# Kernel optimization log

Measured on AMD Instinct MI355X. Metric: run time of the kernel, lower is better.

Reference implementation:

```python
import jax, jax.numpy as jnp
import numpy as np

N = 100000          # nodes
E = 800000          # directed edges (before self-loops)
IN_C = 3
HID = 48            # out_channels per head
HEADS = 4
NUM_LAYERS = 3
NEG_SLOPE = 0.2     # PyG GATv2Conv default negative_slope


def setup_inputs() -> dict:
    key = jax.random.key(0)
    ks = iter(jax.random.split(key, 64))
    inp = {}
    inp["x"] = jax.random.normal(next(ks), (N, IN_C), dtype=jnp.float32)
    inp["edge_index"] = jax.random.randint(next(ks), (2, E), 0, N, dtype=jnp.int32)
    dins = [IN_C] + [HID] * (NUM_LAYERS - 1)
    for l, din in enumerate(dins):
        s = 1.0 / np.sqrt(din)
        inp[f"Wl{l}"] = (jax.random.normal(next(ks), (din, HEADS * HID)) * s).astype(jnp.float32)
        inp[f"bl{l}"] = jnp.zeros((HEADS * HID,), jnp.float32)
        inp[f"Wr{l}"] = (jax.random.normal(next(ks), (din, HEADS * HID)) * s).astype(jnp.float32)
        inp[f"br{l}"] = jnp.zeros((HEADS * HID,), jnp.float32)
        inp[f"att{l}"] = (jax.random.normal(next(ks), (HEADS, HID)) / np.sqrt(HID)).astype(jnp.float32)
        inp[f"b{l}"] = jnp.zeros((HID,), jnp.float32)
    inp["head_w"] = (jax.random.normal(next(ks), (HID, 1)) / np.sqrt(HID)).astype(jnp.float32)
    inp["head_b"] = jnp.full((1,), 0.1, jnp.float32)
    return inp


def _gatv2_layer(x, src, dst, Wl, bl, Wr, br, att, bias):
    # PyG GATv2Conv, concat=False, share_weights=False, eval mode (no dropout).
    # x: [N, din]; src/dst: [E'] with self-loops appended.
    xl = (x @ Wl + bl).reshape(N, HEADS, HID)   # lin_l(x) -> source features
    xr = (x @ Wr + br).reshape(N, HEADS, HID)   # lin_r(x) -> target features
    e = jax.nn.leaky_relu(xl[src] + xr[dst], NEG_SLOPE)      # [E', H, C]
    logits = jnp.einsum('ehc,hc->eh', e, att)                # [E', H]
    # numerically stable per-destination-node softmax over incoming edges
    m = jax.ops.segment_max(logits, dst, num_segments=N)     # [N, H]
    ex = jnp.exp(logits - m[dst])
    denom = jax.ops.segment_sum(ex, dst, num_segments=N)     # [N, H]
    alpha = ex / (denom[dst] + 1e-16)                        # [E', H]
    out = jax.ops.segment_sum(xl[src] * alpha[..., None], dst, num_segments=N)  # [N, H, C]
    return out.mean(axis=1) + bias                           # concat=False -> mean over heads, + bias


def reference(x, edge_index, Wl0, bl0, Wr0, br0, att0, b0,
              Wl1, bl1, Wr1, br1, att1, b1,
              Wl2, bl2, Wr2, br2, att2, b2, head_w, head_b):
    loop = jnp.arange(N, dtype=edge_index.dtype)
    src = jnp.concatenate([edge_index[0], loop])  # add_self_loops=True (PyG default)
    dst = jnp.concatenate([edge_index[1], loop])
    params = [(Wl0, bl0, Wr0, br0, att0, b0),
              (Wl1, bl1, Wr1, br1, att1, b1),
              (Wl2, bl2, Wr2, br2, att2, b2)]
    for p in params:
        x = jax.nn.elu(_gatv2_layer(x, src, dst, *p))  # F.elu; dropout is identity in eval
    out = (x @ head_w + head_b)[:, 0]                  # Linear head, squeeze(-1)
    return jax.nn.softplus(out)                        # output_activation='softplus'
```

## Files before the change

kernel.cpp:

```cpp
#include <hip/hip_runtime.h>
#include <math.h>

#define NN 100000
#define NPAD 100096
#define EE 800000
#define NHEADS 4
#define HID 48
#define FDIM (NHEADS * HID)
#define ROWB 384
#define KPAD 64
#define TLES 4
#define SCAN_CHUNK 2048
#define NBLK ((NN + SCAN_CHUNK - 1) / SCAN_CHUNK)

typedef unsigned int uint;
typedef unsigned short ushort;

#if __has_builtin(__builtin_amdgcn_exp2f)
#define EXP2(x) __builtin_amdgcn_exp2f(x)
#else
#define EXP2(x) exp2f(x)
#endif

struct U3 { uint x, y, z; };

typedef __attribute__((ext_vector_type(8))) short s16x8;
typedef __attribute__((ext_vector_type(4))) float f32x4;


__global__ void hist_k(const int* __restrict__ ei, int* __restrict__ cnt) {
    int e = blockIdx.x * blockDim.x + threadIdx.x;
    if (e >= EE) return;
    atomicAdd(&cnt[ei[EE + e]], 1);
}

__global__ void scan1_k(const int* __restrict__ cnt, int* __restrict__ rowptr,
                        int* __restrict__ bsum) {
    __shared__ int lds[256];
    int b = blockIdx.x, t = threadIdx.x;
    int base = b * SCAN_CHUNK + t * 8;
    int v[8], s = 0;
#pragma unroll
    for (int i = 0; i < 8; i++) { v[i] = (base + i < NN) ? cnt[base + i] : 0; s += v[i]; }
    lds[t] = s;
    __syncthreads();
    for (int off = 1; off < 256; off <<= 1) {
        int val = (t >= off) ? lds[t - off] : 0;
        __syncthreads();
        lds[t] += val;
        __syncthreads();
    }
    if (t == 255) bsum[b] = lds[255];
    int run = lds[t] - s;
#pragma unroll
    for (int i = 0; i < 8; i++) {
        if (base + i < NN) rowptr[base + i] = run;
        run += v[i];
    }
}

__global__ void scan2_k(int* __restrict__ bsum) {
    if (threadIdx.x == 0 && blockIdx.x == 0) {
        int acc = 0;
        for (int b = 0; b < NBLK; b++) { int v = bsum[b]; bsum[b] = acc; acc += v; }
    }
}

__global__ void scan3_k(int* __restrict__ rowptr, const int* __restrict__ bsum,
                        const int* __restrict__ cnt, int2* __restrict__ rc) {
    int i = blockIdx.x * blockDim.x + threadIdx.x;
    if (i < NN) {
        int rp = rowptr[i] + bsum[i / SCAN_CHUNK];
        rowptr[i] = rp;
        rc[i] = make_int2(rp, cnt[i]);
    }
}

__global__ void scatter_k(const int* __restrict__ ei, const int* __restrict__ rowptr,
                          int* __restrict__ fill, int* __restrict__ esrc) {
    int e = blockIdx.x * blockDim.x + threadIdx.x;
    if (e >= EE) return;
    int d = ei[EE + e];
    int pos = rowptr[d] + atomicAdd(&fill[d], 1);
    esrc[pos] = ei[e];
}


__device__ __forceinline__ uint f2bf(float x) {
    uint u = __float_as_uint(x);
    return (u + 0x7FFFu + ((u >> 16) & 1u)) >> 16;
}
__device__ __forceinline__ float bfl(uint u) { return __uint_as_float(u << 16); }
__device__ __forceinline__ float bfh(uint u) { return __uint_as_float(u & 0xFFFF0000u); }

__global__ void wprep_k(const float* __restrict__ Wl1, const float* __restrict__ Wr1,
                        const float* __restrict__ Wl2, const float* __restrict__ Wr2,
                        ushort* __restrict__ Wt1, ushort* __restrict__ Wt2) {
    int t = blockIdx.x * blockDim.x + threadIdx.x;
    if (t >= 2 * KPAD * 384) return;
    int l = t / (KPAD * 384);
    int rem = t - l * (KPAD * 384);
    int k = rem / 384;
    int c = rem - k * 384;
    int cc = (c >= 192) ? c - 192 : c;
    const float* W = (l == 0) ? (c < 192 ? Wl1 : Wr1) : (c < 192 ? Wl2 : Wr2);
    float v = (k < 48) ? W[k * FDIM + cc] : 0.0f;
    uint hi = f2bf(v);
    float lo = v - bfl(hi);
    uint lob = f2bf(lo);
    ushort* Wt = (l == 0) ? Wt1 : Wt2;
    Wt[c * KPAD + k] = (ushort)hi;
    Wt[384 * KPAD + c * KPAD + k] = (ushort)lob;
}

__launch_bounds__(192)
__global__ void gemm2_k(const float* __restrict__ x,
                        const float* __restrict__ Wl, const float* __restrict__ bl,
                        const float* __restrict__ Wr, const float* __restrict__ br,
                        uint* __restrict__ xlb, uint* __restrict__ xrb) {
    const int DIN = 3;
    __shared__ float xs[32][53];
    int t = threadIdx.x;
    int f4 = t % 48, nb = t / 48;
    int node0 = blockIdx.x * 32;

    for (int idx = t; idx < 32 * DIN; idx += 192) {
        int n = idx / DIN, k = idx - n * DIN;
        xs[n][k] = x[(size_t)(node0 + n) * DIN + k];
    }
    __syncthreads();

    float4 accl[8], accr[8];
    {
        float4 bl4 = *(const float4*)(bl + f4 * 4);
        float4 br4 = *(const float4*)(br + f4 * 4);
#pragma unroll
        for (int r = 0; r < 8; r++) { accl[r] = bl4; accr[r] = br4; }
    }

#pragma unroll
    for (int k = 0; k < DIN; k++) {
        float4 wl4 = *(const float4*)(Wl + k * FDIM + f4 * 4);
        float4 wr4 = *(const float4*)(Wr + k * FDIM + f4 * 4);
#pragma unroll
        for (int r = 0; r < 8; r++) {
            float xv = xs[nb * 8 + r][k];
            accl[r].x = fmaf(xv, wl4.x, accl[r].x);
            accl[r].y = fmaf(xv, wl4.y, accl[r].y);
            accl[r].z = fmaf(xv, wl4.z, accl[r].z);
            accl[r].w = fmaf(xv, wl4.w, accl[r].w);
            accr[r].x = fmaf(xv, wr4.x, accr[r].x);
            accr[r].y = fmaf(xv, wr4.y, accr[r].y);
            accr[r].z = fmaf(xv, wr4.z, accr[r].z);
            accr[r].w = fmaf(xv, wr4.w, accr[r].w);
        }
    }

#pragma unroll
    for (int r = 0; r < 8; r++) {
        size_t n = (size_t)node0 + nb * 8 + r;
        uint2 pl, pr;
        pl.x = f2bf(accl[r].x) | (f2bf(accl[r].y) << 16);
        pl.y = f2bf(accl[r].z) | (f2bf(accl[r].w) << 16);
        pr.x = f2bf(accr[r].x) | (f2bf(accr[r].y) << 16);
        pr.y = f2bf(accr[r].z) | (f2bf(accr[r].w) << 16);
        *(uint2*)((char*)xlb + n * ROWB + f4 * 8) = pl;
        *(uint2*)((char*)xrb + n * ROWB + f4 * 8) = pr;
    }
}

__launch_bounds__(256)
__global__ void gemm_mfma_k(const ushort* __restrict__ xbf,
                            const ushort* __restrict__ Wt,
                            const float* __restrict__ bl, const float* __restrict__ br,
                            ushort* __restrict__ xlb, ushort* __restrict__ xrb) {
    __shared__ ushort cs[4][16][104];
    int cg = blockIdx.x & 3;
    int n0 = (blockIdx.x >> 2) * (64 * TLES);
    int wave = threadIdx.x >> 6, lane = threadIdx.x & 63;
    int l15 = lane & 15, l16 = lane >> 4;
    int k8 = l16 * 8;

    s16x8 vbh0[6], vbh1[6], vbl0[6], vbl1[6];
    float bv[6];
#pragma unroll
    for (int ct = 0; ct < 6; ct++) {
        int cglob = cg * 96 + ct * 16 + l15;
        bv[ct] = (cglob < 192) ? bl[cglob] : br[cglob - 192];
        const ushort* bp = Wt + (size_t)cglob * KPAD + k8;
        vbh0[ct] = *(const s16x8*)(bp);
        vbh1[ct] = *(const s16x8*)(bp + 32);
        vbl0[ct] = *(const s16x8*)(bp + 384 * KPAD);
        vbl1[ct] = *(const s16x8*)(bp + 384 * KPAD + 32);
    }

    int colbase = cg * 96;
    ushort* outm = (colbase < 192) ? xlb : xrb;
    int cb = (colbase >= 192) ? colbase - 192 : colbase;

    const ushort* ap = xbf + (size_t)(n0 + wave * 16 + l15) * KPAD + k8;
    s16x8 a0 = *(const s16x8*)(ap);
    s16x8 a1 = *(const s16x8*)(ap + 32);

#pragma unroll
    for (int t = 0; t < TLES; t++) {
        s16x8 na0, na1;
        if (t + 1 < TLES) {
            const ushort* np = ap + (size_t)(t + 1) * 64 * KPAD;
            na0 = *(const s16x8*)(np);
            na1 = *(const s16x8*)(np + 32);
        }
        f32x4 acc[6];
#pragma unroll
        for (int ct = 0; ct < 6; ct++) {
            acc[ct] = (f32x4){bv[ct], bv[ct], bv[ct], bv[ct]};
            acc[ct] = __builtin_amdgcn_mfma_f32_16x16x32_bf16(a0, vbh0[ct], acc[ct], 0, 0, 0);
            acc[ct] = __builtin_amdgcn_mfma_f32_16x16x32_bf16(a1, vbh1[ct], acc[ct], 0, 0, 0);
            acc[ct] = __builtin_amdgcn_mfma_f32_16x16x32_bf16(a0, vbl0[ct], acc[ct], 0, 0, 0);
            acc[ct] = __builtin_amdgcn_mfma_f32_16x16x32_bf16(a1, vbl1[ct], acc[ct], 0, 0, 0);
        }
#pragma unroll
        for (int ct = 0; ct < 6; ct++)
#pragma unroll
            for (int r = 0; r < 4; r++)
                cs[wave][l16 * 4 + r][ct * 16 + l15] = (ushort)f2bf(acc[ct][r]);
        int nb0 = n0 + t * 64 + wave * 16;
#pragma unroll
        for (int i = 0; i < 3; i++) {
            int idx = lane + i * 64;
            int row = idx / 12, q = idx - row * 12;
            int node = nb0 + row;
            if (node < NN) {
                uint4 v = *(const uint4*)(&cs[wave][row][q * 8]);
                *(uint4*)(outm + (size_t)node * FDIM + cb + q * 8) = v;
            }
        }
        if (t + 1 < TLES) { a0 = na0; a1 = na1; }
    }
}

template <int CTRL>
__device__ __forceinline__ float dpp_add(float x) {
    int v = __builtin_amdgcn_update_dpp(0, __float_as_int(x), CTRL, 0xF, 0xF, true);
    return x + __int_as_float(v);
}
__device__ __forceinline__ float red8(float x) {
    x = dpp_add<0x141>(x);
    x = dpp_add<0x04E>(x);
    x = dpp_add<0x0B1>(x);
    return x;
}

#define GAT_PAIR(CU, VALID)                                                      \
    {                                                                            \
        float ca0 = bfl(CU.x), ca1 = bfh(CU.x), ca2 = bfl(CU.y);                 \
        float ca3 = bfh(CU.y), ca4 = bfl(CU.z), ca5 = bfh(CU.z);                 \
        float t0 = ca0 + r0; t0 = fmaxf(t0, 0.2f * t0);                          \
        float t1 = ca1 + r1; t1 = fmaxf(t1, 0.2f * t1);                          \
        float t2 = ca2 + r2; t2 = fmaxf(t2, 0.2f * t2);                          \
        float t3 = ca3 + r3; t3 = fmaxf(t3, 0.2f * t3);                          \
        float t4 = ca4 + r4; t4 = fmaxf(t4, 0.2f * t4);                          \
        float t5 = ca5 + r5; t5 = fmaxf(t5, 0.2f * t5);                          \
        float l = red8(fmaf(t0, w0, fmaf(t1, w1, fmaf(t2, w2,                    \
                       fmaf(t3, w3, fmaf(t4, w4, t5 * w5))))));                  \
        float mn = (VALID) ? fmaxf(m, l) : m;                                    \
        float p = (VALID) ? EXP2(l - mn) : 0.0f;                                 \
        float c = EXP2(m - mn);                                                  \
        s = fmaf(s, c, p);                                                       \
        o0 = fmaf(o0, c, p * ca0);                                               \
        o1 = fmaf(o1, c, p * ca1);                                               \
        o2 = fmaf(o2, c, p * ca2);                                               \
        o3 = fmaf(o3, c, p * ca3);                                               \
        o4 = fmaf(o4, c, p * ca4);                                               \
        o5 = fmaf(o5, c, p * ca5);                                               \
        m = mn;                                                                  \
    }

#define BPERM(K) __builtin_amdgcn_ds_bpermute((((K) & 31) << 3) + half4, my_src)

__global__ void gat_node_k(const uint* __restrict__ xlb, const uint* __restrict__ xrb,
                           const int2* __restrict__ rc, const int* __restrict__ esrc,
                           const float* __restrict__ att, const float* __restrict__ bias,
                           ushort* __restrict__ xbf_out,
                           const float* __restrict__ headw, const float* __restrict__ headb,
                           float* __restrict__ out) {
    int wid = (blockIdx.x * blockDim.x + threadIdx.x) >> 6;
    int lane = threadIdx.x & 63;
    if (wid >= NN) return;
    int d = wid;
    int half = lane >> 5;
    int hb = lane & 31;
    int h = hb >> 3;
    int j = hb & 7;
    int boff = h * 96 + j * 12;
    int half4 = half << 2;

    const float LOG2E = 1.4426950408889634f;
    const float* ap = att + h * HID + j * 6;
    float w0 = ap[0] * LOG2E, w1 = ap[1] * LOG2E, w2 = ap[2] * LOG2E;
    float w3 = ap[3] * LOG2E, w4 = ap[4] * LOG2E, w5 = ap[5] * LOG2E;

    const char* xlc = (const char*)xlb;
    const char* xrc = (const char*)xrb;

    U3 ur = *(const U3*)(xrc + (size_t)d * ROWB + boff);
    float r0 = bfl(ur.x), r1 = bfh(ur.x), r2 = bfl(ur.y);
    float r3 = bfh(ur.y), r4 = bfl(ur.z), r5 = bfh(ur.z);

    U3 us = *(const U3*)(xlc + (size_t)d * ROWB + boff);
    float a0 = bfl(us.x), a1 = bfh(us.x), a2 = bfl(us.y);
    float a3 = bfh(us.y), a4 = bfl(us.z), a5 = bfh(us.z);
    float v0 = a0 + r0; v0 = fmaxf(v0, 0.2f * v0);
    float v1 = a1 + r1; v1 = fmaxf(v1, 0.2f * v1);
    float v2 = a2 + r2; v2 = fmaxf(v2, 0.2f * v2);
    float v3 = a3 + r3; v3 = fmaxf(v3, 0.2f * v3);
    float v4 = a4 + r4; v4 = fmaxf(v4, 0.2f * v4);
    float v5 = a5 + r5; v5 = fmaxf(v5, 0.2f * v5);
    float lself = red8(fmaf(v0, w0, fmaf(v1, w1, fmaf(v2, w2,
                       fmaf(v3, w3, fmaf(v4, w4, v5 * w5))))));

    float m = half ? -3.0e38f : lself;
    float s = half ? 0.0f : 1.0f;
    float o0 = half ? 0.f : a0, o1 = half ? 0.f : a1, o2 = half ? 0.f : a2;
    float o3 = half ? 0.f : a3, o4 = half ? 0.f : a4, o5 = half ? 0.f : a5;

    int2 rcv = rc[d];
    int start = __builtin_amdgcn_readfirstlane(rcv.x);
    int deg = __builtin_amdgcn_readfirstlane(rcv.y);

    for (int cb = 0; cb < deg; cb += 64) {
        int rem = deg - cb; if (rem > 64) rem = 64;
        int my_src = 0;
        if (lane < rem) my_src = esrc[start + cb + lane];
        int npairs = (rem + 1) >> 1;

        int sA = BPERM(0);
        int sB = BPERM(1);
        U3 b0 = *(const U3*)(xlc + (uint)sA * (uint)ROWB + (uint)boff);
        int sC = BPERM(2);
        U3 b1 = *(const U3*)(xlc + (uint)sB * (uint)ROWB + (uint)boff);

#pragma unroll 2
        for (int i = 0; i < npairs - 1; i++) {
            U3 b2 = *(const U3*)(xlc + (uint)sC * (uint)ROWB + (uint)boff);
            sC = BPERM(i + 3);
            GAT_PAIR(b0, true);
            b0 = b1; b1 = b2;
        }
        {
            bool valid = (((npairs - 1) << 1) + half) < rem;
            GAT_PAIR(b0, valid);
        }
    }

    float m2 = __shfl_xor(m, 32);
    float s2 = __shfl_xor(s, 32);
    float mn = fmaxf(m, m2);
    float c1 = EXP2(m - mn), c2 = EXP2(m2 - mn);
    float sm = fmaf(s, c1, s2 * c2);
    float inv = 1.0f / (sm + 1e-16f);
    float q0 = fmaf(o0, c1, __shfl_xor(o0, 32) * c2) * inv;
    float q1 = fmaf(o1, c1, __shfl_xor(o1, 32) * c2) * inv;
    float q2 = fmaf(o2, c1, __shfl_xor(o2, 32) * c2) * inv;
    float q3 = fmaf(o3, c1, __shfl_xor(o3, 32) * c2) * inv;
    float q4 = fmaf(o4, c1, __shfl_xor(o4, 32) * c2) * inv;
    float q5 = fmaf(o5, c1, __shfl_xor(o5, 32) * c2) * inv;

    q0 += __shfl_xor(q0, 8); q0 += __shfl_xor(q0, 16);
    q1 += __shfl_xor(q1, 8); q1 += __shfl_xor(q1, 16);
    q2 += __shfl_xor(q2, 8); q2 += __shfl_xor(q2, 16);
    q3 += __shfl_xor(q3, 8); q3 += __shfl_xor(q3, 16);
    q4 += __shfl_xor(q4, 8); q4 += __shfl_xor(q4, 16);
    q5 += __shfl_xor(q5, 8); q5 += __shfl_xor(q5, 16);

    if (lane < 8) {
        const float* bp = bias + j * 6;
        float y0 = fmaf(q0, 0.25f, bp[0]);
        float y1 = fmaf(q1, 0.25f, bp[1]);
        float y2 = fmaf(q2, 0.25f, bp[2]);
        float y3 = fmaf(q3, 0.25f, bp[3]);
        float y4 = fmaf(q4, 0.25f, bp[4]);
        float y5 = fmaf(q5, 0.25f, bp[5]);
        y0 = y0 > 0.f ? y0 : (EXP2(y0 * LOG2E) - 1.0f);
        y1 = y1 > 0.f ? y1 : (EXP2(y1 * LOG2E) - 1.0f);
        y2 = y2 > 0.f ? y2 : (EXP2(y2 * LOG2E) - 1.0f);
        y3 = y3 > 0.f ? y3 : (EXP2(y3 * LOG2E) - 1.0f);
        y4 = y4 > 0.f ? y4 : (EXP2(y4 * LOG2E) - 1.0f);
        y5 = y5 > 0.f ? y5 : (EXP2(y5 * LOG2E) - 1.0f);
        if (headw) {
            const float* hp = headw + j * 6;
            float pd = fmaf(y0, hp[0], fmaf(y1, hp[1], fmaf(y2, hp[2],
                       fmaf(y3, hp[3], fmaf(y4, hp[4], y5 * hp[5])))));
            pd = red8(pd);
            if (j == 0) {
                float acc = pd + headb[0];
                out[d] = fmaxf(acc, 0.f) + log1pf(expf(-fabsf(acc)));
            }
        } else {
            U3 pk;
            pk.x = f2bf(y0) | (f2bf(y1) << 16);
            pk.y = f2bf(y2) | (f2bf(y3) << 16);
            pk.z = f2bf(y4) | (f2bf(y5) << 16);
            *(U3*)(xbf_out + (size_t)d * KPAD + j * 6) = pk;
        }
    }
}

static inline int cdiv(long a, long b) { return (int)((a + b - 1) / b); }

extern "C" void kernel_launch(void* const* d_in, const int* in_sizes, int n_in,
                              void* d_out, int out_size, void* d_ws, size_t ws_size,
                              hipStream_t stream) {
    const float* x0 = (const float*)d_in[0];
    const int* ei = (const int*)d_in[1];
    const float* Wl[3] = {(const float*)d_in[2], (const float*)d_in[8], (const float*)d_in[14]};
    const float* bl[3] = {(const float*)d_in[3], (const float*)d_in[9], (const float*)d_in[15]};
    const float* Wr[3] = {(const float*)d_in[4], (const float*)d_in[10], (const float*)d_in[16]};
    const float* br[3] = {(const float*)d_in[5], (const float*)d_in[11], (const float*)d_in[17]};
    const float* att[3] = {(const float*)d_in[6], (const float*)d_in[12], (const float*)d_in[18]};
    const float* bb[3] = {(const float*)d_in[7], (const float*)d_in[13], (const float*)d_in[19]};
    const float* hw = (const float*)d_in[20];
    const float* hb = (const float*)d_in[21];

    char* ws = (char*)d_ws;
    uint* xlb = (uint*)ws;      ws += (size_t)NN * ROWB;
    uint* xrb = (uint*)ws;      ws += (size_t)NN * ROWB;
    ushort* xbf = (ushort*)ws;  ws += (size_t)NPAD * KPAD * 2;
    ushort* Wt1 = (ushort*)ws;  ws += (size_t)2 * 384 * KPAD * 2;
    ushort* Wt2 = (ushort*)ws;  ws += (size_t)2 * 384 * KPAD * 2;
    int* rowptr = (int*)ws;     ws += (size_t)NN * 4;
    int* cnt = (int*)ws;        ws += (size_t)NN * 4;
    int* fill = (int*)ws;       ws += (size_t)NN * 4;
    int2* rc = (int2*)ws;       ws += (size_t)NN * 8;
    int* esrc = (int*)ws;       ws += (size_t)EE * 4;
    int* bsum = (int*)ws;       ws += (size_t)NBLK * 4;

    hipMemsetAsync(cnt, 0, (size_t)NN * 4, stream);
    hipMemsetAsync(fill, 0, (size_t)NN * 4, stream);
    hipMemsetAsync(xbf, 0, (size_t)NPAD * KPAD * 2, stream);
    wprep_k<<<cdiv(2 * KPAD * 384, 256), 256, 0, stream>>>(Wl[1], Wr[1], Wl[2], Wr[2], Wt1, Wt2);
    hist_k<<<cdiv(EE, 256), 256, 0, stream>>>(ei, cnt);
    scan1_k<<<NBLK, 256, 0, stream>>>(cnt, rowptr, bsum);
    scan2_k<<<1, 64, 0, stream>>>(bsum);
    scan3_k<<<cdiv(NN, 256), 256, 0, stream>>>(rowptr, bsum, cnt, rc);
    scatter_k<<<cdiv(EE, 256), 256, 0, stream>>>(ei, rowptr, fill, esrc);

    const int GAT_GRID = cdiv((long)NN * 64, 256);
    const int MFMA_GRID = cdiv(NN, 64 * TLES) * 4;

    gemm2_k<<<NN / 32, 192, 0, stream>>>(x0, Wl[0], bl[0], Wr[0], br[0], xlb, xrb);
    gat_node_k<<<GAT_GRID, 256, 0, stream>>>(xlb, xrb, rc, esrc, att[0], bb[0],
                                             xbf, nullptr, nullptr, nullptr);
    gemm_mfma_k<<<MFMA_GRID, 256, 0, stream>>>(xbf, Wt1, bl[1], br[1],
                                               (ushort*)xlb, (ushort*)xrb);
    gat_node_k<<<GAT_GRID, 256, 0, stream>>>(xlb, xrb, rc, esrc, att[1], bb[1],
                                             xbf, nullptr, nullptr, nullptr);
    gemm_mfma_k<<<MFMA_GRID, 256, 0, stream>>>(xbf, Wt2, bl[2], br[2],
                                               (ushort*)xlb, (ushort*)xrb);
    gat_node_k<<<GAT_GRID, 256, 0, stream>>>(xlb, xrb, rc, esrc, att[2], bb[2],
                                             nullptr, hw, hb, (float*)d_out);
}
```

Baseline: 419.9 us.

## Merge setup launches, skip online-softmax rescale when max unchanged, use DPP reductions

Fuses the histogram and weight-prep kernels into one launch, folds the single-thread block-sum scan into scan3, and replaces three memsets with one contiguous memset. This trims launch and small-kernel overhead in CSR setup. In the GAT inner loop, a wave-uniform branch skips the rescale exps when no lane's logit exceeds the running max. The unroll pragma is dropped, and the final cross-lane sums use DPP and swizzle instead of shuffles. The branch adds divergence checks, and dropping the unroll may hurt latency hiding in the loop.

```diff
diff --git a/kernel.cpp b/kernel.cpp
--- a/kernel.cpp
+++ b/kernel.cpp
@@ -12,6 +12,7 @@
 #define TLES 4
 #define SCAN_CHUNK 2048
 #define NBLK ((NN + SCAN_CHUNK - 1) / SCAN_CHUNK)
+#define HIST_BLKS (EE / 256)
 
 typedef unsigned int uint;
 typedef unsigned short ushort;
@@ -28,64 +29,6 @@
 typedef __attribute__((ext_vector_type(4))) float f32x4;
 
 
-__global__ void hist_k(const int* __restrict__ ei, int* __restrict__ cnt) {
-    int e = blockIdx.x * blockDim.x + threadIdx.x;
-    if (e >= EE) return;
-    atomicAdd(&cnt[ei[EE + e]], 1);
-}
-
-__global__ void scan1_k(const int* __restrict__ cnt, int* __restrict__ rowptr,
-                        int* __restrict__ bsum) {
-    __shared__ int lds[256];
-    int b = blockIdx.x, t = threadIdx.x;
-    int base = b * SCAN_CHUNK + t * 8;
-    int v[8], s = 0;
-#pragma unroll
-    for (int i = 0; i < 8; i++) { v[i] = (base + i < NN) ? cnt[base + i] : 0; s += v[i]; }
-    lds[t] = s;
-    __syncthreads();
-    for (int off = 1; off < 256; off <<= 1) {
-        int val = (t >= off) ? lds[t - off] : 0;
-        __syncthreads();
-        lds[t] += val;
-        __syncthreads();
-    }
-    if (t == 255) bsum[b] = lds[255];
-    int run = lds[t] - s;
-#pragma unroll
-    for (int i = 0; i < 8; i++) {
-        if (base + i < NN) rowptr[base + i] = run;
-        run += v[i];
-    }
-}
-
-__global__ void scan2_k(int* __restrict__ bsum) {
-    if (threadIdx.x == 0 && blockIdx.x == 0) {
-        int acc = 0;
-        for (int b = 0; b < NBLK; b++) { int v = bsum[b]; bsum[b] = acc; acc += v; }
-    }
-}
-
-__global__ void scan3_k(int* __restrict__ rowptr, const int* __restrict__ bsum,
-                        const int* __restrict__ cnt, int2* __restrict__ rc) {
-    int i = blockIdx.x * blockDim.x + threadIdx.x;
-    if (i < NN) {
-        int rp = rowptr[i] + bsum[i / SCAN_CHUNK];
-        rowptr[i] = rp;
-        rc[i] = make_int2(rp, cnt[i]);
-    }
-}
-
-__global__ void scatter_k(const int* __restrict__ ei, const int* __restrict__ rowptr,
-                          int* __restrict__ fill, int* __restrict__ esrc) {
-    int e = blockIdx.x * blockDim.x + threadIdx.x;
-    if (e >= EE) return;
-    int d = ei[EE + e];
-    int pos = rowptr[d] + atomicAdd(&fill[d], 1);
-    esrc[pos] = ei[e];
-}
-
-
 __device__ __forceinline__ uint f2bf(float x) {
     uint u = __float_as_uint(x);
     return (u + 0x7FFFu + ((u >> 16) & 1u)) >> 16;
@@ -93,11 +36,18 @@
 __device__ __forceinline__ float bfl(uint u) { return __uint_as_float(u << 16); }
 __device__ __forceinline__ float bfh(uint u) { return __uint_as_float(u & 0xFFFF0000u); }
 
-__global__ void wprep_k(const float* __restrict__ Wl1, const float* __restrict__ Wr1,
-                        const float* __restrict__ Wl2, const float* __restrict__ Wr2,
-                        ushort* __restrict__ Wt1, ushort* __restrict__ Wt2) {
-    int t = blockIdx.x * blockDim.x + threadIdx.x;
-    if (t >= 2 * KPAD * 384) return;
+
+__global__ void histwprep_k(const int* __restrict__ ei, int* __restrict__ cnt,
+                            const float* __restrict__ Wl1, const float* __restrict__ Wr1,
+                            const float* __restrict__ Wl2, const float* __restrict__ Wr2,
+                            ushort* __restrict__ Wt1, ushort* __restrict__ Wt2) {
+    int b = blockIdx.x;
+    if (b < HIST_BLKS) {
+        int e = b * 256 + threadIdx.x;
+        atomicAdd(&cnt[ei[EE + e]], 1);
+        return;
+    }
+    int t = (b - HIST_BLKS) * 256 + threadIdx.x;
     int l = t / (KPAD * 384);
     int rem = t - l * (KPAD * 384);
     int k = rem / 384;
@@ -113,6 +63,59 @@
     Wt[384 * KPAD + c * KPAD + k] = (ushort)lob;
 }
 
+__global__ void scan1_k(const int* __restrict__ cnt, int* __restrict__ rowptr,
+                        int* __restrict__ bsum) {
+    __shared__ int lds[256];
+    int b = blockIdx.x, t = threadIdx.x;
+    int base = b * SCAN_CHUNK + t * 8;
+    int v[8], s = 0;
+#pragma unroll
+    for (int i = 0; i < 8; i++) { v[i] = (base + i < NN) ? cnt[base + i] : 0; s += v[i]; }
+    lds[t] = s;
+    __syncthreads();
+    for (int off = 1; off < 256; off <<= 1) {
+        int val = (t >= off) ? lds[t - off] : 0;
+        __syncthreads();
+        lds[t] += val;
+        __syncthreads();
+    }
+    if (t == 255) bsum[b] = lds[255];
+    int run = lds[t] - s;
+#pragma unroll
+    for (int i = 0; i < 8; i++) {
+        if (base + i < NN) rowptr[base + i] = run;
+        run += v[i];
+    }
+}
+
+__global__ void scan3_k(int* __restrict__ rowptr, const int* __restrict__ bsum,
+                        const int* __restrict__ cnt, int2* __restrict__ rc) {
+    __shared__ int pref[64];
+    int t = threadIdx.x;
+    if (t < 64) pref[t] = (t < NBLK) ? bsum[t] : 0;
+    __syncthreads();
+    if (t == 0) {
+        int acc = 0;
+        for (int b = 0; b < NBLK; b++) { int v = pref[b]; pref[b] = acc; acc += v; }
+    }
+    __syncthreads();
+    int i = blockIdx.x * 256 + t;
+    if (i < NN) {
+        int rp = rowptr[i] + pref[i / SCAN_CHUNK];
+        rowptr[i] = rp;
+        rc[i] = make_int2(rp, cnt[i]);
+    }
+}
+
+__global__ void scatter_k(const int* __restrict__ ei, const int* __restrict__ rowptr,
+                          int* __restrict__ fill, int* __restrict__ esrc) {
+    int e = blockIdx.x * blockDim.x + threadIdx.x;
+    if (e >= EE) return;
+    int d = ei[EE + e];
+    int pos = rowptr[d] + atomicAdd(&fill[d], 1);
+    esrc[pos] = ei[e];
+}
+
 __launch_bounds__(192)
 __global__ void gemm2_k(const float* __restrict__ x,
                         const float* __restrict__ Wl, const float* __restrict__ bl,
@@ -249,6 +252,10 @@
     x = dpp_add<0x04E>(x);
     x = dpp_add<0x0B1>(x);
     return x;
+}
+__device__ __forceinline__ float swz_add16(float x) {
+    int v = __builtin_amdgcn_ds_swizzle(__float_as_int(x), 0x401F);
+    return x + __int_as_float(v);
 }
 
 #define GAT_PAIR(CU, VALID)                                                      \
@@ -263,17 +270,28 @@
         float t5 = ca5 + r5; t5 = fmaxf(t5, 0.2f * t5);                          \
         float l = red8(fmaf(t0, w0, fmaf(t1, w1, fmaf(t2, w2,                    \
                        fmaf(t3, w3, fmaf(t4, w4, t5 * w5))))));                  \
-        float mn = (VALID) ? fmaxf(m, l) : m;                                    \
-        float p = (VALID) ? EXP2(l - mn) : 0.0f;                                 \
-        float c = EXP2(m - mn);                                                  \
-        s = fmaf(s, c, p);                                                       \
-        o0 = fmaf(o0, c, p * ca0);                                               \
-        o1 = fmaf(o1, c, p * ca1);                                               \
-        o2 = fmaf(o2, c, p * ca2);                                               \
-        o3 = fmaf(o3, c, p * ca3);                                               \
-        o4 = fmaf(o4, c, p * ca4);                                               \
-        o5 = fmaf(o5, c, p * ca5);                                               \
-        m = mn;                                                                  \
+        if (__all((l <= m) | (int)!(VALID))) {                                   \
+            float p = (VALID) ? EXP2(l - m) : 0.0f;                              \
+            s += p;                                                              \
+            o0 = fmaf(p, ca0, o0);                                               \
+            o1 = fmaf(p, ca1, o1);                                               \
+            o2 = fmaf(p, ca2, o2);                                               \
+            o3 = fmaf(p, ca3, o3);                                               \
+            o4 = fmaf(p, ca4, o4);                                               \
+            o5 = fmaf(p, ca5, o5);                                               \
+        } else {                                                                 \
+            float mn = (VALID) ? fmaxf(m, l) : m;                                \
+            float p = (VALID) ? EXP2(l - mn) : 0.0f;                             \
+            float c = EXP2(m - mn);                                              \
+            s = fmaf(s, c, p);                                                   \
+            o0 = fmaf(o0, c, p * ca0);                                           \
+            o1 = fmaf(o1, c, p * ca1);                                           \
+            o2 = fmaf(o2, c, p * ca2);                                           \
+            o3 = fmaf(o3, c, p * ca3);                                           \
+            o4 = fmaf(o4, c, p * ca4);                                           \
+            o5 = fmaf(o5, c, p * ca5);                                           \
+            m = mn;                                                              \
+        }                                                                        \
     }
 
 #define BPERM(K) __builtin_amdgcn_ds_bpermute((((K) & 31) << 3) + half4, my_src)
@@ -340,7 +358,6 @@
         int sC = BPERM(2);
         U3 b1 = *(const U3*)(xlc + (uint)sB * (uint)ROWB + (uint)boff);
 
-#pragma unroll 2
         for (int i = 0; i < npairs - 1; i++) {
             U3 b2 = *(const U3*)(xlc + (uint)sC * (uint)ROWB + (uint)boff);
             sC = BPERM(i + 3);
@@ -366,12 +383,12 @@
     float q4 = fmaf(o4, c1, __shfl_xor(o4, 32) * c2) * inv;
     float q5 = fmaf(o5, c1, __shfl_xor(o5, 32) * c2) * inv;
 
-    q0 += __shfl_xor(q0, 8); q0 += __shfl_xor(q0, 16);
-    q1 += __shfl_xor(q1, 8); q1 += __shfl_xor(q1, 16);
-    q2 += __shfl_xor(q2, 8); q2 += __shfl_xor(q2, 16);
-    q3 += __shfl_xor(q3, 8); q3 += __shfl_xor(q3, 16);
-    q4 += __shfl_xor(q4, 8); q4 += __shfl_xor(q4, 16);
-    q5 += __shfl_xor(q5, 8); q5 += __shfl_xor(q5, 16);
+    q0 = dpp_add<0x128>(q0); q0 = swz_add16(q0);
+    q1 = dpp_add<0x128>(q1); q1 = swz_add16(q1);
+    q2 = dpp_add<0x128>(q2); q2 = swz_add16(q2);
+    q3 = dpp_add<0x128>(q3); q3 = swz_add16(q3);
+    q4 = dpp_add<0x128>(q4); q4 = swz_add16(q4);
+    q5 = dpp_add<0x128>(q5); q5 = swz_add16(q5);
 
     if (lane < 8) {
         const float* bp = bias + j * 6;
@@ -425,23 +442,21 @@
     char* ws = (char*)d_ws;
     uint* xlb = (uint*)ws;      ws += (size_t)NN * ROWB;
     uint* xrb = (uint*)ws;      ws += (size_t)NN * ROWB;
-    ushort* xbf = (ushort*)ws;  ws += (size_t)NPAD * KPAD * 2;
     ushort* Wt1 = (ushort*)ws;  ws += (size_t)2 * 384 * KPAD * 2;
     ushort* Wt2 = (ushort*)ws;  ws += (size_t)2 * 384 * KPAD * 2;
     int* rowptr = (int*)ws;     ws += (size_t)NN * 4;
-    int* cnt = (int*)ws;        ws += (size_t)NN * 4;
-    int* fill = (int*)ws;       ws += (size_t)NN * 4;
     int2* rc = (int2*)ws;       ws += (size_t)NN * 8;
     int* esrc = (int*)ws;       ws += (size_t)EE * 4;
     int* bsum = (int*)ws;       ws += (size_t)NBLK * 4;
-
-    hipMemsetAsync(cnt, 0, (size_t)NN * 4, stream);
-    hipMemsetAsync(fill, 0, (size_t)NN * 4, stream);
-    hipMemsetAsync(xbf, 0, (size_t)NPAD * KPAD * 2, stream);
-    wprep_k<<<cdiv(2 * KPAD * 384, 256), 256, 0, stream>>>(Wl[1], Wr[1], Wl[2], Wr[2], Wt1, Wt2);
-    hist_k<<<cdiv(EE, 256), 256, 0, stream>>>(ei, cnt);
+    int* cnt = (int*)ws;        ws += (size_t)NN * 4;
+    int* fill = (int*)ws;       ws += (size_t)NN * 4;
+    ushort* xbf = (ushort*)ws;  ws += (size_t)NPAD * KPAD * 2;
+    const size_t ZBYTES = (size_t)NN * 4 * 2 + (size_t)NPAD * KPAD * 2;
+
+    hipMemsetAsync(cnt, 0, ZBYTES, stream);
+    histwprep_k<<<HIST_BLKS + (2 * KPAD * 384) / 256, 256, 0, stream>>>(
+        ei, cnt, Wl[1], Wr[1], Wl[2], Wr[2], Wt1, Wt2);
     scan1_k<<<NBLK, 256, 0, stream>>>(cnt, rowptr, bsum);
-    scan2_k<<<1, 64, 0, stream>>>(bsum);
     scan3_k<<<cdiv(NN, 256), 256, 0, stream>>>(rowptr, bsum, cnt, rc);
     scatter_k<<<cdiv(EE, 256), 256, 0, stream>>>(ei, rowptr, fill, esrc);
 
```

New measurement: 414.2 us (median of 2 runs). Within noise of the previous version (-1.4%).
